# Kernel optimization log

Hardware: AMD Instinct MI355X
Metric: run time of the kernel (lower is better)

The kernel has to match this reference:

```python
import jax, jax.numpy as jnp
import numpy as np

DIM = 512
HEADS = 8
DIM_HEAD = 64
INNER = HEADS * DIM_HEAD  # 512
SCALE = DIM_HEAD ** -0.5


def setup_inputs() -> dict:
    key = jax.random.key(0)
    k1, k2, k3, k4 = jax.random.split(key, 4)
    x = jax.random.normal(k1, (4, 2048, DIM), dtype=jnp.float32)
    # Dense(inner_dim*3, use_bias=False): weight [dim, 3*inner]
    w_qkv = jax.random.normal(k2, (DIM, 3 * INNER), dtype=jnp.float32) * (DIM ** -0.5)
    # to_out Dense(dim): weight [inner, dim] + bias [dim]
    w_out = jax.random.normal(k3, (INNER, DIM), dtype=jnp.float32) * (INNER ** -0.5)
    b_out = jax.random.normal(k4, (DIM,), dtype=jnp.float32) * 0.01
    return {"x": x, "w_qkv": w_qkv, "w_out": w_out, "b_out": b_out}


def reference(x, w_qkv, w_out, b_out):
    b, n, _ = x.shape
    qkv = x @ w_qkv                                  # [b, n, 3*inner]
    q, k, v = jnp.split(qkv, 3, axis=-1)             # each [b, n, inner]
    def to_heads(t):
        return t.reshape(b, n, HEADS, DIM_HEAD).transpose(0, 2, 1, 3)  # [b, h, n, d]
    q, k, v = map(to_heads, (q, k, v))
    dots = jnp.einsum('bhid,bhjd->bhij', q, k) * SCALE
    attn = jax.nn.softmax(dots, axis=-1)
    out = jnp.einsum('bhij,bhjd->bhid', attn, v)     # [b, h, n, d]
    out = out.transpose(0, 2, 1, 3).reshape(b, n, INNER)
    return out @ w_out + b_out                       # [b, n, dim]
```

## Files before the change

### kernel.cpp

```cpp
#include <hip/hip_runtime.h>
#include <stdint.h>

#define DIM    512
#define HEADS  8
#define DHEAD  64
#define SEQ    2048
#define BATCH  4
#define BH     (BATCH*HEADS)
#define MROWS  (BATCH*SEQ)
#define NQKV   (3*DIM)
#define QSCALE 0.18033688011112042f

typedef __bf16 bf16x8 __attribute__((ext_vector_type(8)));
typedef float  f32x4  __attribute__((ext_vector_type(4)));
typedef float  f32x16 __attribute__((ext_vector_type(16)));

typedef unsigned short u16;

#if __has_builtin(__builtin_amdgcn_exp2f)
#define EXP2(x) __builtin_amdgcn_exp2f(x)
#else
#define EXP2(x) exp2f(x)
#endif

__device__ __forceinline__ u16 f2bf(float f) {
    union { float f; uint32_t u; } v; v.f = f;
    uint32_t u = v.u;
    uint32_t r = (u + 0x7FFFu + ((u >> 16) & 1u)) >> 16;
    return (u16)r;
}
__device__ __forceinline__ float bf2f(u16 h) {
    union { uint32_t u; float f; } v; v.u = ((uint32_t)h) << 16;
    return v.f;
}
__device__ __forceinline__ uint32_t pk2bf(float a, float b) {
    union { float f; uint32_t u; } ua, ub; ua.f = a; ub.f = b;
#if __has_builtin(__builtin_amdgcn_perm)
    return __builtin_amdgcn_perm(ub.u + 0x8000u, ua.u + 0x8000u, 0x07060302u);
#else
    return ((ua.u + 0x8000u) >> 16) | ((ub.u + 0x8000u) & 0xFFFF0000u);
#endif
}

#define P32SWAP(x, y) asm("v_permlane32_swap_b32 %0, %1" : "+v"(x), "+v"(y))

__device__ __forceinline__ void async16(const void* g, u16* l) {
    __builtin_amdgcn_global_load_lds(
        (const __attribute__((address_space(1))) void*)g,
        (__attribute__((address_space(3))) void*)l, 16, 0, 0);
}

#define XBLKS (MROWS * DIM / 4 / 256)
#define WQT   ((DIM / 64) * (NQKV / 64))
#define WOT   ((DIM / 64) * (DIM / 64))
__global__ void prep(const void* __restrict__ x, const void* __restrict__ wq,
                     const void* __restrict__ wo, u16* __restrict__ xb,
                     u16* __restrict__ wtq, u16* __restrict__ wto,
                     int* __restrict__ flag) {
    __shared__ int cnt;
    __shared__ __align__(16) u16 tile[64][72];
    int tid = threadIdx.x;
    if (tid == 0) cnt = 0;
    __syncthreads();
    {
        u16 v = ((const u16*)x)[tid * 2];
        int e = (v >> 7) & 0xFF;
        atomicAdd(&cnt, (v == 0) || (e >= 100 && e <= 140));
    }
    __syncthreads();
    int isbf = (cnt >= 192);
    int b = blockIdx.x;
    if (b == 0 && tid == 0) *flag = isbf;

    if (b < XBLKS) {
        int i = b * 256 + tid;
        if (isbf) {
            ((uint2*)xb)[i] = ((const uint2*)x)[i];
        } else {
            float4 v = ((const float4*)x)[i];
            ushort4 o;
            o.x = f2bf(v.x); o.y = f2bf(v.y); o.z = f2bf(v.z); o.w = f2bf(v.w);
            ((ushort4*)xb)[i] = o;
        }
        return;
    }
    const void* W; u16* Wt; int N, tb;
    if (b < XBLKS + WQT) { W = wq; Wt = wtq; N = NQKV; tb = b - XBLKS; }
    else                 { W = wo; Wt = wto; N = DIM;  tb = b - XBLKS - WQT; }
    int tn = N / 64;
    int k0 = (tb / tn) * 64, n0 = (tb - (tb / tn) * tn) * 64;

#pragma unroll 4
    for (int it = 0; it < 16; ++it) {
        int idx = it * 256 + tid;
        int r = idx >> 6, c = idx & 63;
        u16 v = isbf ? ((const u16*)W)[(size_t)(k0 + r) * N + n0 + c]
                     : f2bf(((const float*)W)[(size_t)(k0 + r) * N + n0 + c]);
        tile[c][r] = v;
    }
    __syncthreads();
    {
        int n = tid >> 2, ks = (tid & 3) * 16;
        uint4 v0 = *(const uint4*)&tile[n][ks];
        uint4 v1 = *(const uint4*)&tile[n][ks + 8];
        *(uint4*)&Wt[(size_t)(n0 + n) * DIM + k0 + ks] = v0;
        *(uint4*)&Wt[(size_t)(n0 + n) * DIM + k0 + ks + 8] = v1;
    }
}

template<int KDIM, int TM, int TN>
__device__ __forceinline__ void gemm_lds_db(
        const u16* __restrict__ A, const u16* __restrict__ Bt,
        int m0, int n0, int tid, u16* As, u16* Bs,
        f32x4 (&acc)[TM / 32][TN / 32]) {
    int lane = tid & 63, ln = lane & 15, quad = lane >> 4, w = tid >> 6;
    int wm = (w >> 1) * (TM / 2), wn = (w & 1) * (TN / 2);

    auto stage = [&](int buf, int k0) {
#pragma unroll
        for (int ii = 0; ii < TM / 64; ++ii) {
            int r0 = (ii * 4 + w) * 16;
            int row = r0 + (lane >> 2);
            int seg = (lane & 3) ^ (row & 3);
            async16(A + (size_t)(m0 + row) * KDIM + k0 + seg * 8,
                    As + buf * TM * 32 + r0 * 32);
        }
#pragma unroll
        for (int ii = 0; ii < TN / 64; ++ii) {
            int r0 = (ii * 4 + w) * 16;
            int row = r0 + (lane >> 2);
            int seg = (lane & 3) ^ (row & 3);
            async16(Bt + (size_t)(n0 + row) * KDIM + k0 + seg * 8,
                    Bs + buf * TN * 32 + r0 * 32);
        }
    };

    stage(0, 0);
#pragma unroll 1
    for (int kk = 0; kk < KDIM / 32; ++kk) {
        __syncthreads();
        if (kk + 1 < KDIM / 32) stage((kk + 1) & 1, (kk + 1) * 32);
        const u16* Ac = As + (kk & 1) * TM * 32;
        const u16* Bc = Bs + (kk & 1) * TN * 32;
        bf16x8 a[TM / 32], b[TN / 32];
        int rseg = (quad ^ (ln & 3)) * 8;
#pragma unroll
        for (int i = 0; i < TM / 32; ++i)
            a[i] = *(const bf16x8*)(Ac + (wm + i * 16 + ln) * 32 + rseg);
#pragma unroll
        for (int j = 0; j < TN / 32; ++j)
            b[j] = *(const bf16x8*)(Bc + (wn + j * 16 + ln) * 32 + rseg);
#pragma unroll
        for (int i = 0; i < TM / 32; ++i)
#pragma unroll
            for (int j = 0; j < TN / 32; ++j)
                acc[i][j] = __builtin_amdgcn_mfma_f32_16x16x32_bf16(
                    a[i], b[j], acc[i][j], 0, 0, 0);
    }
}

__global__ __launch_bounds__(256, 3) void qkv_gemm(
        const u16* __restrict__ X, const u16* __restrict__ Wt,
        u16* __restrict__ Qt, u16* __restrict__ Kb, u16* __restrict__ Vt) {
    __shared__ __align__(16) u16 As[2 * 128 * 32];
    __shared__ __align__(16) u16 Bs[2 * 128 * 32];

    int tid  = threadIdx.x;
    int lane = tid & 63, ln = lane & 15, quad = lane >> 4, wid = tid >> 6;
    int m0 = blockIdx.x * 128, n0 = blockIdx.y * 128;
    int wm = (wid >> 1) * 64, wn = (wid & 1) * 64;

    f32x4 acc[4][4];
#pragma unroll
    for (int i = 0; i < 4; ++i)
#pragma unroll
        for (int j = 0; j < 4; ++j) acc[i][j] = 0.f;

    gemm_lds_db<DIM, 128, 128>(X, Wt, m0, n0, tid, As, Bs, acc);

#pragma unroll
    for (int j = 0; j < 4; ++j) {
        int col   = n0 + wn + j * 16 + ln;
        int which = col >> 9;
        int hd    = col & 511;
        int h     = hd >> 6, d = hd & 63;
#pragma unroll
        for (int i = 0; i < 4; ++i) {
            int rbase = m0 + wm + i * 16 + quad * 4;
            int b = rbase >> 11, n = rbase & 2047;
            int bh = b * HEADS + h;
            if (which == 1) {
#pragma unroll
                for (int r = 0; r < 4; ++r)
                    Kb[((size_t)bh * SEQ + n + r) * DHEAD + d] = f2bf(acc[i][j][r]);
            } else {
                float s = (which == 0) ? QSCALE : 1.0f;
                uint2 pv;
                pv.x = pk2bf(acc[i][j][0] * s, acc[i][j][1] * s);
                pv.y = pk2bf(acc[i][j][2] * s, acc[i][j][3] * s);
                u16* dst = (which == 0) ? Qt : Vt;
                *(uint2*)&dst[((size_t)bh * DHEAD + d) * SEQ + n] = pv;
            }
        }
    }
}

__global__ __launch_bounds__(512, 4) void flash_attn(
        const u16* __restrict__ Qt, const u16* __restrict__ Kb,
        const u16* __restrict__ Vt, u16* __restrict__ Ob) {
    __shared__ __align__(16) u16 SMEM[18432];
    __shared__ float Lcomb[4][32];
    __shared__ float Lq[4][32];
    u16* Kc0 = SMEM;
    u16* Vc0 = SMEM + 8192;
    float* OC = (float*)SMEM;

    int tid  = threadIdx.x;
    int lane = tid & 63, c = lane & 31, hi = lane >> 5, wid = tid >> 6;
    int ws = wid & 1, wq = wid >> 1;
    int bh = blockIdx.x;
    int q0 = blockIdx.y * 128 + wq * 32;

    const u16* Qh = Qt + (size_t)bh * SEQ * DHEAD;
    const u16* Kh = Kb + (size_t)bh * SEQ * DHEAD;
    const u16* Vh = Vt + (size_t)bh * DHEAD * SEQ;

    int srow = lane >> 3;
    auto stageKV = [&](int buf, int kc) {
        int slab = wid;
        int g = (lane & 7) ^ srow ^ (slab & 3);
        const u16* gk = Kh + (size_t)(kc + slab * 8 + srow) * DHEAD + g * 8;
        async16(gk, Kc0 + buf * 4096 + slab * 8 * 64);
        const u16* gv = Vh + (size_t)(slab * 8 + srow) * SEQ + kc + g * 8;
        async16(gv, Vc0 + buf * 4096 + slab * 8 * 64);
    };

    bf16x8 qf[4];
#pragma unroll
    for (int ds = 0; ds < 4; ++ds) {
        union { u16 a[8]; bf16x8 v; } u;
#pragma unroll
        for (int j = 0; j < 8; ++j)
            u.a[j] = Qh[(size_t)(ds * 16 + hi * 8 + j) * SEQ + q0 + c];
        qf[ds] = u.v;
    }

    f32x16 o[2];
    float lsum = 0.f;
#pragma unroll
    for (int dt = 0; dt < 2; ++dt) o[dt] = 0.f;

    stageKV(0, 0);
    __syncthreads();

    int fl = (c & 7) ^ ((c >> 3) & 3);

#pragma unroll 1
    for (int kc = 0; kc < SEQ; kc += 64) {
        int cur = (kc >> 6) & 1;
        if (kc + 64 < SEQ) stageKV(cur ^ 1, kc + 64);

        const u16* Kcur = Kc0 + cur * 4096;
        const u16* Vcur = Vc0 + cur * 4096;

        bf16x8 kf[4];
#pragma unroll
        for (int ds = 0; ds < 4; ++ds) {
            int slot = (ds * 2 + hi) ^ fl;
            kf[ds] = *(const bf16x8*)&Kcur[(ws * 32 + c) * 64 + slot * 8];
        }

        f32x16 s;
        s = 0.f;
        __builtin_amdgcn_s_setprio(1);
#pragma unroll
        for (int ds = 0; ds < 4; ++ds)
            s = __builtin_amdgcn_mfma_f32_32x32x16_bf16(
                kf[ds], qf[ds], s, 0, 0, 0);
        __builtin_amdgcn_s_setprio(0);

        float p[16];
#pragma unroll
        for (int r = 0; r < 16; ++r) p[r] = EXP2(s[r]);
        {
            float t0 = (p[0] + p[1]) + (p[2] + p[3]);
            float t1 = (p[4] + p[5]) + (p[6] + p[7]);
            float t2 = (p[8] + p[9]) + (p[10] + p[11]);
            float t3 = (p[12] + p[13]) + (p[14] + p[15]);
            lsum += (t0 + t1) + (t2 + t3);
        }
        uint32_t X[8];
#pragma unroll
        for (int i = 0; i < 8; ++i) X[i] = pk2bf(p[2 * i], p[2 * i + 1]);
        P32SWAP(X[0], X[2]); P32SWAP(X[1], X[3]);
        P32SWAP(X[4], X[6]); P32SWAP(X[5], X[7]);
        bf16x8 pa[2];
        union { uint32_t d[4]; bf16x8 v; } u0, u1;
        u0.d[0] = X[0]; u0.d[1] = X[1]; u0.d[2] = X[2]; u0.d[3] = X[3];
        u1.d[0] = X[4]; u1.d[1] = X[5]; u1.d[2] = X[6]; u1.d[3] = X[7];
        pa[0] = u0.v; pa[1] = u1.v;

        __builtin_amdgcn_s_setprio(1);
#pragma unroll
        for (int tl = 0; tl < 2; ++tl)
#pragma unroll
            for (int dt = 0; dt < 2; ++dt) {
                int slot = ((ws * 2 + tl) * 2 + hi) ^ fl;
                bf16x8 vf = *(const bf16x8*)&Vcur[(dt * 32 + c) * 64 + slot * 8];
                o[dt] = __builtin_amdgcn_mfma_f32_32x32x16_bf16(
                    pa[tl], vf, o[dt], 0, 0, 0);
            }
        __builtin_amdgcn_s_setprio(0);

        __syncthreads();
    }

    lsum += __shfl_xor(lsum, 32);

    if (ws == 1) {
#pragma unroll
        for (int dt = 0; dt < 2; ++dt) {
            int base = (((wq * 2 + dt) * 2 + hi) * 32 + c) * 18;
#pragma unroll
            for (int g = 0; g < 4; ++g) {
                f32x4 v;
                v[0] = o[dt][g * 4 + 0]; v[1] = o[dt][g * 4 + 1];
                v[2] = o[dt][g * 4 + 2]; v[3] = o[dt][g * 4 + 3];
                *(f32x4*)&OC[base + g * 4] = v;
            }
        }
        if (hi == 0) Lcomb[wq][c] = lsum;
    }
    __syncthreads();
    if (ws == 0) {
#pragma unroll
        for (int dt = 0; dt < 2; ++dt) {
            int base = (((wq * 2 + dt) * 2 + hi) * 32 + c) * 18;
#pragma unroll
            for (int g = 0; g < 4; ++g) {
                f32x4 v = *(const f32x4*)&OC[base + g * 4];
                o[dt][g * 4 + 0] += v[0]; o[dt][g * 4 + 1] += v[1];
                o[dt][g * 4 + 2] += v[2]; o[dt][g * 4 + 3] += v[3];
            }
        }
        float ltot = lsum + Lcomb[wq][c];
        if (hi == 0) Lq[wq][c] = ltot;
    }
    __syncthreads();

    if (ws == 0) {
        int b = bh >> 3, hh = bh & 7;
        f32x16 linv;
#pragma unroll
        for (int r = 0; r < 16; ++r)
            linv[r] = 1.0f / Lq[wq][(r & 3) + 8 * (r >> 2) + 4 * hi];
#pragma unroll
        for (int dt = 0; dt < 2; ++dt)
#pragma unroll
            for (int r = 0; r < 16; ++r) {
                int ql = (r & 3) + 8 * (r >> 2) + 4 * hi;
                int n  = q0 + ql;
                int d  = dt * 32 + c;
                Ob[((size_t)(b * SEQ + n)) * DIM + hh * DHEAD + d] =
                    f2bf(o[dt][r] * linv[r]);
            }
    }
}

__global__ __launch_bounds__(256, 3) void out_gemm(
        const u16* __restrict__ A, const u16* __restrict__ Wt,
        const void* __restrict__ bias, void* __restrict__ out,
        const int* __restrict__ flag) {
    __shared__ __align__(16) u16 As[2 * 64 * 32];
    __shared__ __align__(16) u16 Bs[2 * 128 * 32];

    int tid  = threadIdx.x;
    int lane = tid & 63, ln = lane & 15, quad = lane >> 4, wid = tid >> 6;
    int m0 = blockIdx.x * 64, n0 = blockIdx.y * 128;
    int wm = (wid >> 1) * 32, wn = (wid & 1) * 64;
    int isbf = *flag;

    f32x4 acc[2][4];
#pragma unroll
    for (int i = 0; i < 2; ++i)
#pragma unroll
        for (int j = 0; j < 4; ++j) acc[i][j] = 0.f;

    gemm_lds_db<DIM, 64, 128>(A, Wt, m0, n0, tid, As, Bs, acc);

#pragma unroll
    for (int j = 0; j < 4; ++j) {
        int col = n0 + wn + j * 16 + ln;
        float bv = isbf ? bf2f(((const u16*)bias)[col])
                        : ((const float*)bias)[col];
#pragma unroll
        for (int i = 0; i < 2; ++i) {
            int rbase = m0 + wm + i * 16 + quad * 4;
#pragma unroll
            for (int r = 0; r < 4; ++r) {
                int row = rbase + r;
                size_t off = (size_t)row * DIM + col;
                float val = acc[i][j][r] + bv;
                if (isbf) ((u16*)out)[off] = f2bf(val);
                else      ((float*)out)[off] = val;
            }
        }
    }
}

extern "C" void kernel_launch(void* const* d_in, const int* in_sizes, int n_in,
                              void* d_out, int out_size, void* d_ws, size_t ws_size,
                              hipStream_t stream) {
    const void* x     = d_in[0];
    const void* w_qkv = d_in[1];
    const void* w_out = d_in[2];
    const void* b_out = d_in[3];

    int* flag   = (int*)d_ws;
    u16* x_bf   = (u16*)((char*)d_ws + 16);
    u16* wt_qkv = x_bf + (size_t)MROWS * DIM;
    u16* wt_out = wt_qkv + (size_t)NQKV * DIM;
    u16* Qt     = wt_out + (size_t)DIM * DIM;
    u16* Kb     = Qt + (size_t)BH * SEQ * DHEAD;
    u16* Vt     = Kb + (size_t)BH * SEQ * DHEAD;
    u16* attn   = x_bf;

    prep<<<XBLKS + WQT + WOT, 256, 0, stream>>>(
        x, w_qkv, w_out, x_bf, wt_qkv, wt_out, flag);
    qkv_gemm<<<dim3(MROWS / 128, NQKV / 128), 256, 0, stream>>>(x_bf, wt_qkv, Qt, Kb, Vt);
    flash_attn<<<dim3(BH, SEQ / 128), 512, 0, stream>>>(Qt, Kb, Vt, attn);
    out_gemm<<<dim3(MROWS / 64, DIM / 128), 256, 0, stream>>>(attn, wt_out, b_out, d_out, flag);
}
```

Before: 176.3 us.

## Triple-buffer KV staging with one barrier, MFMA row sums, hardware bf16 pack

The flash attention loop moves from double to triple buffering of K/V tiles in LDS. It uses explicit vmcnt waits and a single s_barrier per iteration instead of a trailing __syncthreads, so loads are issued two tiles ahead. The softmax denominator is now accumulated by an extra MFMA against a ones vector rather than scalar adds. This removes the final reduction stage and one block barrier. The bf16 packing uses the v_cvt_pk_bf16_f32 instruction, and LDS use grows, which may lower occupancy.

Result: no change. 178.1 us (+1.1%).

```diff
diff --git a/kernel.cpp b/kernel.cpp
--- a/kernel.cpp
+++ b/kernel.cpp
@@ -40,6 +40,11 @@
 #else
     return ((ua.u + 0x8000u) >> 16) | ((ub.u + 0x8000u) & 0xFFFF0000u);
 #endif
+}
+__device__ __forceinline__ uint32_t cvtpk(float a, float b) {
+    uint32_t r;
+    asm("v_cvt_pk_bf16_f32 %0, %1, %2" : "=v"(r) : "v"(a), "v"(b));
+    return r;
 }
 
 #define P32SWAP(x, y) asm("v_permlane32_swap_b32 %0, %1" : "+v"(x), "+v"(y))
@@ -208,11 +213,10 @@
 __global__ __launch_bounds__(512, 4) void flash_attn(
         const u16* __restrict__ Qt, const u16* __restrict__ Kb,
         const u16* __restrict__ Vt, u16* __restrict__ Ob) {
-    __shared__ __align__(16) u16 SMEM[18432];
+    __shared__ __align__(16) u16 SMEM[24576];
     __shared__ float Lcomb[4][32];
-    __shared__ float Lq[4][32];
     u16* Kc0 = SMEM;
-    u16* Vc0 = SMEM + 8192;
+    u16* Vc0 = SMEM + 12288;
     float* OC = (float*)SMEM;
 
     int tid  = threadIdx.x;
@@ -245,20 +249,29 @@
         qf[ds] = u.v;
     }
 
+    bf16x8 onesf;
+    { union { uint32_t d[4]; bf16x8 v; } u;
+      u.d[0] = u.d[1] = u.d[2] = u.d[3] = 0x3F803F80u; onesf = u.v; }
+
     f32x16 o[2];
-    float lsum = 0.f;
+    f32x16 lacc;
+    lacc = 0.f;
 #pragma unroll
     for (int dt = 0; dt < 2; ++dt) o[dt] = 0.f;
 
     stageKV(0, 0);
-    __syncthreads();
+    stageKV(1, 64);
 
     int fl = (c & 7) ^ ((c >> 3) & 3);
+    int cur = 0;
 
 #pragma unroll 1
     for (int kc = 0; kc < SEQ; kc += 64) {
-        int cur = (kc >> 6) & 1;
-        if (kc + 64 < SEQ) stageKV(cur ^ 1, kc + 64);
+        if (kc + 64 < SEQ) asm volatile("s_waitcnt vmcnt(2)" ::: "memory");
+        else               asm volatile("s_waitcnt vmcnt(0)" ::: "memory");
+        __builtin_amdgcn_s_barrier();
+        __builtin_amdgcn_sched_barrier(0);
+        if (kc + 128 < SEQ) stageKV((cur + 2) % 3, kc + 128);
 
         const u16* Kcur = Kc0 + cur * 4096;
         const u16* Vcur = Vc0 + cur * 4096;
@@ -282,16 +295,9 @@
         float p[16];
 #pragma unroll
         for (int r = 0; r < 16; ++r) p[r] = EXP2(s[r]);
-        {
-            float t0 = (p[0] + p[1]) + (p[2] + p[3]);
-            float t1 = (p[4] + p[5]) + (p[6] + p[7]);
-            float t2 = (p[8] + p[9]) + (p[10] + p[11]);
-            float t3 = (p[12] + p[13]) + (p[14] + p[15]);
-            lsum += (t0 + t1) + (t2 + t3);
-        }
         uint32_t X[8];
 #pragma unroll
-        for (int i = 0; i < 8; ++i) X[i] = pk2bf(p[2 * i], p[2 * i + 1]);
+        for (int i = 0; i < 8; ++i) X[i] = cvtpk(p[2 * i], p[2 * i + 1]);
         P32SWAP(X[0], X[2]); P32SWAP(X[1], X[3]);
         P32SWAP(X[4], X[6]); P32SWAP(X[5], X[7]);
         bf16x8 pa[2];
@@ -302,7 +308,7 @@
 
         __builtin_amdgcn_s_setprio(1);
 #pragma unroll
-        for (int tl = 0; tl < 2; ++tl)
+        for (int tl = 0; tl < 2; ++tl) {
 #pragma unroll
             for (int dt = 0; dt < 2; ++dt) {
                 int slot = ((ws * 2 + tl) * 2 + hi) ^ fl;
@@ -310,12 +316,15 @@
                 o[dt] = __builtin_amdgcn_mfma_f32_32x32x16_bf16(
                     pa[tl], vf, o[dt], 0, 0, 0);
             }
+            lacc = __builtin_amdgcn_mfma_f32_32x32x16_bf16(
+                pa[tl], onesf, lacc, 0, 0, 0);
+        }
         __builtin_amdgcn_s_setprio(0);
 
-        __syncthreads();
-    }
-
-    lsum += __shfl_xor(lsum, 32);
+        cur = (cur == 2) ? 0 : cur + 1;
+    }
+
+    __syncthreads();
 
     if (ws == 1) {
 #pragma unroll
@@ -329,10 +338,16 @@
                 *(f32x4*)&OC[base + g * 4] = v;
             }
         }
-        if (hi == 0) Lcomb[wq][c] = lsum;
+        if (c == 0) {
+#pragma unroll
+            for (int r = 0; r < 16; ++r)
+                Lcomb[wq][(r & 3) + 8 * (r >> 2) + 4 * hi] = lacc[r];
+        }
     }
     __syncthreads();
+
     if (ws == 0) {
+        int b = bh >> 3, hh = bh & 7;
 #pragma unroll
         for (int dt = 0; dt < 2; ++dt) {
             int base = (((wq * 2 + dt) * 2 + hi) * 32 + c) * 18;
@@ -343,17 +358,10 @@
                 o[dt][g * 4 + 2] += v[2]; o[dt][g * 4 + 3] += v[3];
             }
         }
-        float ltot = lsum + Lcomb[wq][c];
-        if (hi == 0) Lq[wq][c] = ltot;
-    }
-    __syncthreads();
-
-    if (ws == 0) {
-        int b = bh >> 3, hh = bh & 7;
         f32x16 linv;
 #pragma unroll
         for (int r = 0; r < 16; ++r)
-            linv[r] = 1.0f / Lq[wq][(r & 3) + 8 * (r >> 2) + 4 * hi];
+            linv[r] = 1.0f / (lacc[r] + Lcomb[wq][(r & 3) + 8 * (r >> 2) + 4 * hi]);
 #pragma unroll
         for (int dt = 0; dt < 2; ++dt)
 #pragma unroll
```
